# Kernel optimization log

Measured on AMD Instinct MI355X. Metric: run time of the kernel, lower is better.

The kernel has to match this reference:

```python
import jax, jax.numpy as jnp
import numpy as np

N_SRC = 50000
N_DST1 = 20000
N_DST2 = 10000
E1 = 320000
E2 = 160000
T = 12
C_IN = 64
HID = 16
C_OUT = 32


def _gat_layer(src_feat, dst_feat, src_idx, dst_idx, ew, W, a_l, a_r, n_dst):
    # src_feat: [N_src, T, C], dst_feat: [N_dst, T, C]
    h_src = jnp.einsum('ntc,co->nto', src_feat, W)   # [N_src, T, O]
    h_dst = jnp.einsum('ntc,co->nto', dst_feat, W)   # [N_dst, T, O]
    el = jnp.einsum('nto,o->nt', h_src, a_l)          # [N_src, T]
    er = jnp.einsum('nto,o->nt', h_dst, a_r)          # [N_dst, T]
    # per-edge attention logits
    e = jax.nn.leaky_relu(el[src_idx] + er[dst_idx], negative_slope=0.2)  # [E, T]
    # segment softmax over incoming edges of each dst node
    m = jax.ops.segment_max(e, dst_idx, num_segments=n_dst)               # [N_dst, T]
    ex = jnp.exp(e - m[dst_idx])
    s = jax.ops.segment_sum(ex, dst_idx, num_segments=n_dst)
    alpha = ex / (s[dst_idx] + 1e-9)                                      # [E, T]
    msg = (alpha * ew[:, None])[:, :, None] * h_src[src_idx]              # [E, T, O]
    return jax.ops.segment_sum(msg, dst_idx, num_segments=n_dst)          # [N_dst, T, O]


def setup_inputs() -> dict:
    key = jax.random.key(0)
    ks = jax.random.split(key, 12)
    inp = {
        'node_feat': jax.random.normal(ks[0], (T, N_SRC, C_IN), dtype=jnp.float32),
        'edge_src1': jax.random.randint(ks[1], (E1,), 0, N_SRC, dtype=jnp.int32),
        'edge_dst1': jax.random.randint(ks[2], (E1,), 0, N_DST1, dtype=jnp.int32),
        'edge_weight1': jax.random.uniform(ks[3], (E1,), dtype=jnp.float32),
        'edge_src2': jax.random.randint(ks[4], (E2,), 0, N_DST1, dtype=jnp.int32),
        'edge_dst2': jax.random.randint(ks[5], (E2,), 0, N_DST2, dtype=jnp.int32),
        'edge_weight2': jax.random.uniform(ks[6], (E2,), dtype=jnp.float32),
        'W1': jax.random.normal(ks[7], (C_IN, HID), dtype=jnp.float32) * (1.0 / np.sqrt(C_IN)),
        'a_l1': jax.random.normal(ks[8], (HID,), dtype=jnp.float32) * 0.1,
        'a_r1': jax.random.normal(ks[9], (HID,), dtype=jnp.float32) * 0.1,
        'W2': jax.random.normal(ks[10], (HID, C_OUT), dtype=jnp.float32) * (1.0 / np.sqrt(HID)),
        'a_l2': jax.random.normal(ks[11], (C_OUT,), dtype=jnp.float32) * 0.1,
        'a_r2': jax.random.normal(jax.random.fold_in(key, 99), (C_OUT,), dtype=jnp.float32) * 0.1,
    }
    return inp


def reference(node_feat, edge_src1, edge_dst1, edge_weight1,
              edge_src2, edge_dst2, edge_weight2,
              W1, a_l1, a_r1, W2, a_l2, a_r2):
    # [T, N, C] -> [N, T, C]
    x = jnp.transpose(node_feat, (1, 0, 2))
    h1 = _gat_layer(x, x[:N_DST1], edge_src1, edge_dst1, edge_weight1,
                    W1, a_l1, a_r1, N_DST1)
    h1 = jax.nn.leaky_relu(h1, negative_slope=0.01)
    h2 = _gat_layer(h1, h1[:N_DST2], edge_src2, edge_dst2, edge_weight2,
                    W2, a_l2, a_r2, N_DST2)
    h2 = jax.nn.leaky_relu(h2, negative_slope=0.01)
    # [N_dst2, T, O] -> [T, N_dst2, O]
    return jnp.transpose(h2, (1, 0, 2))
```

## Files before the change

### kernel.cpp

```cpp
#include <hip/hip_runtime.h>

#define N_SRC 50000
#define N_DST1 20000
#define N_DST2 10000
#define E1 320000
#define E2 160000
#define T 12
#define C_IN 64
#define HID 16
#define C_OUT 32

__device__ __forceinline__ float lrelu(float x, float s) { return x > 0.f ? x : s * x; }

__device__ __forceinline__ int xcd_swizzle(int p, int W) {
    int x = p & 7, k = p >> 3;
    int q = W >> 3, r = W & 7;
    return (x < r ? x * (q + 1) : r * (q + 1) + (x - r) * q) + k;
}

__global__ __launch_bounds__(256) void k_zero(int4* __restrict__ p, int n4)
{
    int i = blockIdx.x * 256 + threadIdx.x;
    if (i < n4) p[i] = make_int4(0, 0, 0, 0);
}

__global__ __launch_bounds__(256) void k_transform1(
    const float* __restrict__ nf, const float* __restrict__ W1,
    const float* __restrict__ a_l, const float* __restrict__ a_r,
    float* __restrict__ hs1, float* __restrict__ el1, float* __restrict__ er1)
{
    __shared__ float xs[64][68];
    __shared__ float w[C_IN][HID];
    __shared__ float al[HID], ar[HID];
    int tx = threadIdx.x;
    int t = blockIdx.y;
    int n0 = blockIdx.x * 64;
    int nrem = N_SRC - n0; if (nrem > 64) nrem = 64;

    reinterpret_cast<float4*>(&w[0][0])[tx] = reinterpret_cast<const float4*>(W1)[tx];
    if (tx < HID) al[tx] = a_l[tx];
    else if (tx < 2 * HID) ar[tx - HID] = a_r[tx - HID];

    const float4* gp = reinterpret_cast<const float4*>(nf + ((size_t)t * N_SRC + n0) * C_IN);
#pragma unroll
    for (int k = 0; k < 4; k++) {
        int f = k * 256 + tx;
        int node = f >> 4;
        if (node < nrem)
            *reinterpret_cast<float4*>(&xs[node][(f & 15) * 4]) = gp[f];
    }
    __syncthreads();

    int q = tx & 3;
    int nn = tx >> 2;
    float4 acc = make_float4(0.f, 0.f, 0.f, 0.f);
#pragma unroll
    for (int c4 = 0; c4 < 16; c4++) {
        float4 xA = *reinterpret_cast<const float4*>(&xs[nn][c4 * 4]);
        float4 w0 = *reinterpret_cast<const float4*>(&w[c4 * 4 + 0][q * 4]);
        float4 w1 = *reinterpret_cast<const float4*>(&w[c4 * 4 + 1][q * 4]);
        float4 w2 = *reinterpret_cast<const float4*>(&w[c4 * 4 + 2][q * 4]);
        float4 w3 = *reinterpret_cast<const float4*>(&w[c4 * 4 + 3][q * 4]);
        acc.x += xA.x * w0.x + xA.y * w1.x + xA.z * w2.x + xA.w * w3.x;
        acc.y += xA.x * w0.y + xA.y * w1.y + xA.z * w2.y + xA.w * w3.y;
        acc.z += xA.x * w0.z + xA.y * w1.z + xA.z * w2.z + xA.w * w3.z;
        acc.w += xA.x * w0.w + xA.y * w1.w + xA.z * w2.w + xA.w * w3.w;
    }

    float el = acc.x * al[q * 4] + acc.y * al[q * 4 + 1] + acc.z * al[q * 4 + 2] + acc.w * al[q * 4 + 3];
    float er = acc.x * ar[q * 4] + acc.y * ar[q * 4 + 1] + acc.z * ar[q * 4 + 2] + acc.w * ar[q * 4 + 3];
    el += __shfl_xor(el, 1); el += __shfl_xor(el, 2);
    er += __shfl_xor(er, 1); er += __shfl_xor(er, 2);

    if (nn < nrem) {
        float* hb = hs1 + ((size_t)t * N_SRC + n0) * HID;
        *reinterpret_cast<float4*>(hb + (size_t)nn * HID + q * 4) = acc;
        if (q == 0) {
            int n = n0 + nn;
            el1[(size_t)t * N_SRC + n] = el;
            if (n < N_DST1) er1[(size_t)t * N_DST1 + n] = er;
        }
    }
}

__global__ __launch_bounds__(256) void k_hist(
    const int* __restrict__ d1, const int* __restrict__ d2,
    int* __restrict__ cnt1, int* __restrict__ cnt2)
{
    int e = blockIdx.x * 256 + threadIdx.x;
    if (e < E1) atomicAdd(&cnt1[d1[e]], 1);
    else if (e < E1 + E2) atomicAdd(&cnt2[d2[e - E1]], 1);
}

__device__ void scan_one(const int* cnt, int* off, int* cur, int N)
{
    __shared__ int part[1024];
    int tx = threadIdx.x;
    int CH = (N + 1023) / 1024;
    int base = tx * CH;
    int p = 0;
    for (int k = 0; k < CH; k++) { int i = base + k; if (i < N) p += cnt[i]; }
    part[tx] = p;
    __syncthreads();
#pragma unroll
    for (int d = 1; d < 1024; d <<= 1) {
        int v = (tx >= d) ? part[tx - d] : 0;
        __syncthreads();
        part[tx] += v;
        __syncthreads();
    }
    int run = (tx == 0) ? 0 : part[tx - 1];
    if (tx == 0) off[0] = 0;
    for (int k = 0; k < CH; k++) {
        int i = base + k;
        if (i < N) { cur[i] = run; run += cnt[i]; off[i + 1] = run; }
    }
}

__global__ __launch_bounds__(1024) void k_scan(
    const int* __restrict__ cnt1, int* __restrict__ off1, int* __restrict__ cur1,
    const int* __restrict__ cnt2, int* __restrict__ off2, int* __restrict__ cur2,
    const float* __restrict__ W2, const float* __restrict__ al2,
    const float* __restrict__ ar2, float* __restrict__ wl2, float* __restrict__ wr2)
{
    if (blockIdx.x == 2) {
        int tx = threadIdx.x;
        if (tx < 32) {
            int c = tx & 15;
            const float* a = (tx < 16) ? al2 : ar2;
            float s = 0.f;
            for (int o = 0; o < C_OUT; o++) s += W2[c * C_OUT + o] * a[o];
            if (tx < 16) wl2[c] = s; else wr2[c] = s;
        }
        return;
    }
    if (blockIdx.x == 0) scan_one(cnt1, off1, cur1, N_DST1);
    else                 scan_one(cnt2, off2, cur2, N_DST2);
}

__global__ __launch_bounds__(256) void k_scatter(
    const int* __restrict__ s1, const int* __restrict__ d1, const float* __restrict__ w1,
    int* __restrict__ cur1, int2* __restrict__ sw1,
    const int* __restrict__ s2, const int* __restrict__ d2, const float* __restrict__ w2,
    int* __restrict__ cur2, int2* __restrict__ sw2)
{
    int e = blockIdx.x * 256 + threadIdx.x;
    if (e < E1) {
        int d = d1[e];
        int p = atomicAdd(&cur1[d], 1);
        sw1[p] = make_int2(s1[e], __float_as_int(w1[e]));
    } else if (e < E1 + E2) {
        int ee = e - E1;
        int d = d2[ee];
        int p = atomicAdd(&cur2[d], 1);
        sw2[p] = make_int2(s2[ee], __float_as_int(w2[ee]));
    }
}

template <int NDST, int NSRC, bool FINAL>
__global__ __launch_bounds__(256) void k_gat(
    const int* __restrict__ off, const int2* __restrict__ sw,
    const float* __restrict__ el, const float* __restrict__ er,
    const float* __restrict__ hs, float* __restrict__ outp,
    const float* __restrict__ wl, const float* __restrict__ wr,
    float* __restrict__ el_out, float* __restrict__ er_out)
{
    __shared__ float w2s[FINAL ? HID * C_OUT : 1];
    int tx = threadIdx.x;
    if (FINAL) {
        for (int idx = tx; idx < HID * C_OUT; idx += 256) w2s[idx] = wl[idx];
        __syncthreads();
    }
    int wblk = xcd_swizzle(blockIdx.x, (NDST * T) / 16);
    int grp = tx >> 4;
    int lane16 = tx & 15;
    int q = lane16 & 3;
    int eslot = lane16 >> 2;
    int g = wblk * 16 + grp;
    int t = g / NDST;
    int d = g - t * NDST;
    int start = off[d], end = off[d + 1];
    float erv = er[g];
    const float* elb = el + (size_t)t * NSRC;
    const float* hsb = hs + (size_t)t * NSRC * HID;

    float4 num = make_float4(0.f, 0.f, 0.f, 0.f);
    float den = 0.f;
    int i = start + eslot;
    for (; i + 4 < end; i += 8) {
        int2 sa = sw[i];
        int2 sb = sw[i + 4];
        float ea = elb[sa.x];
        float eb = elb[sb.x];
        float4 ha = *reinterpret_cast<const float4*>(hsb + (size_t)sa.x * HID + q * 4);
        float4 hb = *reinterpret_cast<const float4*>(hsb + (size_t)sb.x * HID + q * 4);
        float exa = __expf(lrelu(ea + erv, 0.2f));
        float exb = __expf(lrelu(eb + erv, 0.2f));
        den += exa + exb;
        float ca = exa * __int_as_float(sa.y);
        float cb = exb * __int_as_float(sb.y);
        num.x += ca * ha.x + cb * hb.x;
        num.y += ca * ha.y + cb * hb.y;
        num.z += ca * ha.z + cb * hb.z;
        num.w += ca * ha.w + cb * hb.w;
    }
    if (i < end) {
        int2 sa = sw[i];
        float ea = elb[sa.x];
        float4 ha = *reinterpret_cast<const float4*>(hsb + (size_t)sa.x * HID + q * 4);
        float exa = __expf(lrelu(ea + erv, 0.2f));
        den += exa;
        float ca = exa * __int_as_float(sa.y);
        num.x += ca * ha.x; num.y += ca * ha.y;
        num.z += ca * ha.z; num.w += ca * ha.w;
    }
#pragma unroll
    for (int mk = 4; mk <= 8; mk <<= 1) {
        num.x += __shfl_xor(num.x, mk);
        num.y += __shfl_xor(num.y, mk);
        num.z += __shfl_xor(num.z, mk);
        num.w += __shfl_xor(num.w, mk);
        den   += __shfl_xor(den, mk);
    }
    float inv = 1.f / (den + 1e-9f);
    float4 v = make_float4(num.x * inv, num.y * inv, num.z * inv, num.w * inv);

    if (!FINAL) {
        v.x = lrelu(v.x, 0.01f); v.y = lrelu(v.y, 0.01f);
        v.z = lrelu(v.z, 0.01f); v.w = lrelu(v.w, 0.01f);
        if (eslot == 0) {
            *reinterpret_cast<float4*>(outp + (size_t)g * HID + q * 4) = v;
            float pl = v.x * wl[q * 4] + v.y * wl[q * 4 + 1] + v.z * wl[q * 4 + 2] + v.w * wl[q * 4 + 3];
            float pr = v.x * wr[q * 4] + v.y * wr[q * 4 + 1] + v.z * wr[q * 4 + 2] + v.w * wr[q * 4 + 3];
            pl += __shfl_xor(pl, 1); pl += __shfl_xor(pl, 2);
            pr += __shfl_xor(pr, 1); pr += __shfl_xor(pr, 2);
            if (q == 0) {
                el_out[g] = pl;
                if (d < N_DST2) er_out[(size_t)t * N_DST2 + d] = pr;
            }
        }
    } else {
        float4 v1, v2, v3;
        v1.x = __shfl_xor(v.x, 1); v1.y = __shfl_xor(v.y, 1); v1.z = __shfl_xor(v.z, 1); v1.w = __shfl_xor(v.w, 1);
        v2.x = __shfl_xor(v.x, 2); v2.y = __shfl_xor(v.y, 2); v2.z = __shfl_xor(v.z, 2); v2.w = __shfl_xor(v.w, 2);
        v3.x = __shfl_xor(v.x, 3); v3.y = __shfl_xor(v.y, 3); v3.z = __shfl_xor(v.z, 3); v3.w = __shfl_xor(v.w, 3);
        int obase = q * 8;
        float out8[8];
#pragma unroll
        for (int oo = 0; oo < 8; oo++) out8[oo] = 0.f;
#define ACCQ(Q, R0)                                                             \
        {                                                                       \
            int r0 = (R0) * 4;                                                  \
            _Pragma("unroll")                                                   \
            for (int oo = 0; oo < 8; oo++)                                      \
                out8[oo] += (Q).x * w2s[(r0 + 0) * C_OUT + obase + oo]          \
                          + (Q).y * w2s[(r0 + 1) * C_OUT + obase + oo]          \
                          + (Q).z * w2s[(r0 + 2) * C_OUT + obase + oo]          \
                          + (Q).w * w2s[(r0 + 3) * C_OUT + obase + oo];         \
        }
        ACCQ(v,  q);
        ACCQ(v1, q ^ 1);
        ACCQ(v2, q ^ 2);
        ACCQ(v3, q ^ 3);
#undef ACCQ
        if (eslot == 0) {
            float* op = outp + (size_t)g * C_OUT + obase;
            float4 w0 = make_float4(lrelu(out8[0], 0.01f), lrelu(out8[1], 0.01f),
                                    lrelu(out8[2], 0.01f), lrelu(out8[3], 0.01f));
            float4 w1 = make_float4(lrelu(out8[4], 0.01f), lrelu(out8[5], 0.01f),
                                    lrelu(out8[6], 0.01f), lrelu(out8[7], 0.01f));
            *reinterpret_cast<float4*>(op) = w0;
            *reinterpret_cast<float4*>(op + 4) = w1;
        }
    }
}

extern "C" void kernel_launch(void* const* d_in, const int* in_sizes, int n_in,
                              void* d_out, int out_size, void* d_ws, size_t ws_size,
                              hipStream_t stream)
{
    const float* node_feat = (const float*)d_in[0];
    const int*   esrc1     = (const int*)d_in[1];
    const int*   edst1     = (const int*)d_in[2];
    const float* ew1       = (const float*)d_in[3];
    const int*   esrc2     = (const int*)d_in[4];
    const int*   edst2     = (const int*)d_in[5];
    const float* ew2       = (const float*)d_in[6];
    const float* W1        = (const float*)d_in[7];
    const float* a_l1      = (const float*)d_in[8];
    const float* a_r1      = (const float*)d_in[9];
    const float* W2        = (const float*)d_in[10];
    const float* a_l2      = (const float*)d_in[11];
    const float* a_r2      = (const float*)d_in[12];
    float* out = (float*)d_out;

    float* ws = (float*)d_ws;
    float* hs1 = ws;
    float* el1 = hs1 + 9600000;
    float* er1 = el1 + 600000;
    float* h1  = er1 + 240000;
    float* el2 = h1 + 3840000;
    float* er2 = el2 + 240000;
    float* wl2 = er2 + 120000;
    float* wr2 = wl2 + 16;
    int2* sw1 = (int2*)(wr2 + 16);
    int2* sw2 = sw1 + E1;
    int* cnt1 = (int*)(sw2 + E2);
    int* cnt2 = cnt1 + N_DST1;
    int* off1 = cnt2 + N_DST2;
    int* cur1 = off1 + N_DST1 + 1;
    int* off2 = cur1 + N_DST1;
    int* cur2 = off2 + N_DST2 + 1;

    k_zero<<<30, 256, 0, stream>>>((int4*)cnt1, (N_DST1 + N_DST2) / 4);
    k_hist<<<(E1 + E2 + 255) / 256, 256, 0, stream>>>(edst1, edst2, cnt1, cnt2);
    k_scan<<<3, 1024, 0, stream>>>(cnt1, off1, cur1, cnt2, off2, cur2,
                                   W2, a_l2, a_r2, wl2, wr2);
    k_scatter<<<(E1 + E2 + 255) / 256, 256, 0, stream>>>(
        esrc1, edst1, ew1, cur1, sw1,
        esrc2, edst2, ew2, cur2, sw2);

    {
        dim3 g((N_SRC + 63) / 64, T);
        k_transform1<<<g, 256, 0, stream>>>(node_feat, W1, a_l1, a_r1, hs1, el1, er1);
    }
    k_gat<N_DST1, N_SRC, false><<<(N_DST1 * T) / 16, 256, 0, stream>>>(
        off1, sw1, el1, er1, hs1, h1, wl2, wr2, el2, er2);
    k_gat<N_DST2, N_DST1, true><<<(N_DST2 * T) / 16, 256, 0, stream>>>(
        off2, sw2, el2, er2, h1, out, W2, nullptr, nullptr, nullptr);
}
```

Before: 209.2 us.

## Co-schedule transform tiles with histogram and scatter kernels, unroll GAT edge loop

Splits the per-time-step input transform across the histogram and scatter launches, so that half the time steps run as extra blocks alongside each latency-bound atomic pass and the standalone transform launch is removed. The GAT aggregation loop also gains a 4-edge-per-iteration unrolled main loop, which puts more independent gather loads in flight per lane. Mixing block types within one launch may unbalance scheduling, and the wider unroll raises register pressure.

After: 211.6 us. Within noise of the previous version (+1.1%).

```diff
diff --git a/kernel.cpp b/kernel.cpp
--- a/kernel.cpp
+++ b/kernel.cpp
@@ -9,6 +9,8 @@
 #define C_IN 64
 #define HID 16
 #define C_OUT 32
+#define EB 1875
+#define TB 782
 
 __device__ __forceinline__ float lrelu(float x, float s) { return x > 0.f ? x : s * x; }
 
@@ -24,7 +26,8 @@
     if (i < n4) p[i] = make_int4(0, 0, 0, 0);
 }
 
-__global__ __launch_bounds__(256) void k_transform1(
+__device__ __forceinline__ void transform_tile(
+    int nblk, int t, int tx,
     const float* __restrict__ nf, const float* __restrict__ W1,
     const float* __restrict__ a_l, const float* __restrict__ a_r,
     float* __restrict__ hs1, float* __restrict__ el1, float* __restrict__ er1)
@@ -32,9 +35,7 @@
     __shared__ float xs[64][68];
     __shared__ float w[C_IN][HID];
     __shared__ float al[HID], ar[HID];
-    int tx = threadIdx.x;
-    int t = blockIdx.y;
-    int n0 = blockIdx.x * 64;
+    int n0 = nblk * 64;
     int nrem = N_SRC - n0; if (nrem > 64) nrem = 64;
 
     reinterpret_cast<float4*>(&w[0][0])[tx] = reinterpret_cast<const float4*>(W1)[tx];
@@ -83,13 +84,50 @@
     }
 }
 
-__global__ __launch_bounds__(256) void k_hist(
+__global__ __launch_bounds__(256) void k_A(
     const int* __restrict__ d1, const int* __restrict__ d2,
-    int* __restrict__ cnt1, int* __restrict__ cnt2)
-{
-    int e = blockIdx.x * 256 + threadIdx.x;
-    if (e < E1) atomicAdd(&cnt1[d1[e]], 1);
-    else if (e < E1 + E2) atomicAdd(&cnt2[d2[e - E1]], 1);
+    int* __restrict__ cnt1, int* __restrict__ cnt2,
+    const float* __restrict__ nf, const float* __restrict__ W1,
+    const float* __restrict__ a_l, const float* __restrict__ a_r,
+    float* __restrict__ hs1, float* __restrict__ el1, float* __restrict__ er1)
+{
+    if (blockIdx.x < EB) {
+        int e = blockIdx.x * 256 + threadIdx.x;
+        if (e < E1) atomicAdd(&cnt1[d1[e]], 1);
+        else atomicAdd(&cnt2[d2[e - E1]], 1);
+        return;
+    }
+    int idx = blockIdx.x - EB;
+    transform_tile(idx % TB, idx / TB, threadIdx.x,
+                   nf, W1, a_l, a_r, hs1, el1, er1);
+}
+
+__global__ __launch_bounds__(256) void k_B(
+    const int* __restrict__ s1, const int* __restrict__ d1, const float* __restrict__ w1,
+    int* __restrict__ cur1, int2* __restrict__ sw1,
+    const int* __restrict__ s2, const int* __restrict__ d2, const float* __restrict__ w2,
+    int* __restrict__ cur2, int2* __restrict__ sw2,
+    const float* __restrict__ nf, const float* __restrict__ W1,
+    const float* __restrict__ a_l, const float* __restrict__ a_r,
+    float* __restrict__ hs1, float* __restrict__ el1, float* __restrict__ er1)
+{
+    if (blockIdx.x < EB) {
+        int e = blockIdx.x * 256 + threadIdx.x;
+        if (e < E1) {
+            int d = d1[e];
+            int p = atomicAdd(&cur1[d], 1);
+            sw1[p] = make_int2(s1[e], __float_as_int(w1[e]));
+        } else {
+            int ee = e - E1;
+            int d = d2[ee];
+            int p = atomicAdd(&cur2[d], 1);
+            sw2[p] = make_int2(s2[ee], __float_as_int(w2[ee]));
+        }
+        return;
+    }
+    int idx = blockIdx.x - EB;
+    transform_tile(idx % TB, 6 + idx / TB, threadIdx.x,
+                   nf, W1, a_l, a_r, hs1, el1, er1);
 }
 
 __device__ void scan_one(const int* cnt, int* off, int* cur, int N)
@@ -138,24 +176,17 @@
     else                 scan_one(cnt2, off2, cur2, N_DST2);
 }
 
-__global__ __launch_bounds__(256) void k_scatter(
-    const int* __restrict__ s1, const int* __restrict__ d1, const float* __restrict__ w1,
-    int* __restrict__ cur1, int2* __restrict__ sw1,
-    const int* __restrict__ s2, const int* __restrict__ d2, const float* __restrict__ w2,
-    int* __restrict__ cur2, int2* __restrict__ sw2)
-{
-    int e = blockIdx.x * 256 + threadIdx.x;
-    if (e < E1) {
-        int d = d1[e];
-        int p = atomicAdd(&cur1[d], 1);
-        sw1[p] = make_int2(s1[e], __float_as_int(w1[e]));
-    } else if (e < E1 + E2) {
-        int ee = e - E1;
-        int d = d2[ee];
-        int p = atomicAdd(&cur2[d], 1);
-        sw2[p] = make_int2(s2[ee], __float_as_int(w2[ee]));
-    }
-}
+#define EDGE1(I)                                                                \
+    {                                                                           \
+        int2 sa = sw[I];                                                        \
+        float ea = elb[sa.x];                                                   \
+        float4 ha = *reinterpret_cast<const float4*>(hsb + (size_t)sa.x * HID + q * 4); \
+        float exa = __expf(lrelu(ea + erv, 0.2f));                              \
+        den += exa;                                                             \
+        float ca = exa * __int_as_float(sa.y);                                  \
+        num.x += ca * ha.x; num.y += ca * ha.y;                                 \
+        num.z += ca * ha.z; num.w += ca * ha.w;                                 \
+    }
 
 template <int NDST, int NSRC, bool FINAL>
 __global__ __launch_bounds__(256) void k_gat(
@@ -187,6 +218,33 @@
     float4 num = make_float4(0.f, 0.f, 0.f, 0.f);
     float den = 0.f;
     int i = start + eslot;
+    for (; i + 12 < end; i += 16) {
+        int2 sa = sw[i];
+        int2 sb = sw[i + 4];
+        int2 sc = sw[i + 8];
+        int2 sd = sw[i + 12];
+        float ea = elb[sa.x];
+        float eb = elb[sb.x];
+        float ec = elb[sc.x];
+        float ed = elb[sd.x];
+        float4 ha = *reinterpret_cast<const float4*>(hsb + (size_t)sa.x * HID + q * 4);
+        float4 hb = *reinterpret_cast<const float4*>(hsb + (size_t)sb.x * HID + q * 4);
+        float4 hc = *reinterpret_cast<const float4*>(hsb + (size_t)sc.x * HID + q * 4);
+        float4 hd = *reinterpret_cast<const float4*>(hsb + (size_t)sd.x * HID + q * 4);
+        float exa = __expf(lrelu(ea + erv, 0.2f));
+        float exb = __expf(lrelu(eb + erv, 0.2f));
+        float exc = __expf(lrelu(ec + erv, 0.2f));
+        float exd = __expf(lrelu(ed + erv, 0.2f));
+        den += (exa + exb) + (exc + exd);
+        float ca = exa * __int_as_float(sa.y);
+        float cb = exb * __int_as_float(sb.y);
+        float cc = exc * __int_as_float(sc.y);
+        float cd = exd * __int_as_float(sd.y);
+        num.x += ca * ha.x + cb * hb.x + cc * hc.x + cd * hd.x;
+        num.y += ca * ha.y + cb * hb.y + cc * hc.y + cd * hd.y;
+        num.z += ca * ha.z + cb * hb.z + cc * hc.z + cd * hd.z;
+        num.w += ca * ha.w + cb * hb.w + cc * hc.w + cd * hd.w;
+    }
     for (; i + 4 < end; i += 8) {
         int2 sa = sw[i];
         int2 sb = sw[i + 4];
@@ -204,16 +262,7 @@
         num.z += ca * ha.z + cb * hb.z;
         num.w += ca * ha.w + cb * hb.w;
     }
-    if (i < end) {
-        int2 sa = sw[i];
-        float ea = elb[sa.x];
-        float4 ha = *reinterpret_cast<const float4*>(hsb + (size_t)sa.x * HID + q * 4);
-        float exa = __expf(lrelu(ea + erv, 0.2f));
-        den += exa;
-        float ca = exa * __int_as_float(sa.y);
-        num.x += ca * ha.x; num.y += ca * ha.y;
-        num.z += ca * ha.z; num.w += ca * ha.w;
-    }
+    if (i < end) EDGE1(i);
 #pragma unroll
     for (int mk = 4; mk <= 8; mk <<= 1) {
         num.x += __shfl_xor(num.x, mk);
@@ -313,17 +362,13 @@
     int* cur2 = off2 + N_DST2 + 1;
 
     k_zero<<<30, 256, 0, stream>>>((int4*)cnt1, (N_DST1 + N_DST2) / 4);
-    k_hist<<<(E1 + E2 + 255) / 256, 256, 0, stream>>>(edst1, edst2, cnt1, cnt2);
+    k_A<<<EB + TB * 6, 256, 0, stream>>>(edst1, edst2, cnt1, cnt2,
+                                         node_feat, W1, a_l1, a_r1, hs1, el1, er1);
     k_scan<<<3, 1024, 0, stream>>>(cnt1, off1, cur1, cnt2, off2, cur2,
                                    W2, a_l2, a_r2, wl2, wr2);
-    k_scatter<<<(E1 + E2 + 255) / 256, 256, 0, stream>>>(
-        esrc1, edst1, ew1, cur1, sw1,
-        esrc2, edst2, ew2, cur2, sw2);
-
-    {
-        dim3 g((N_SRC + 63) / 64, T);
-        k_transform1<<<g, 256, 0, stream>>>(node_feat, W1, a_l1, a_r1, hs1, el1, er1);
-    }
+    k_B<<<EB + TB * 6, 256, 0, stream>>>(esrc1, edst1, ew1, cur1, sw1,
+                                         esrc2, edst2, ew2, cur2, sw2,
+                                         node_feat, W1, a_l1, a_r1, hs1, el1, er1);
     k_gat<N_DST1, N_SRC, false><<<(N_DST1 * T) / 16, 256, 0, stream>>>(
         off1, sw1, el1, er1, hs1, h1, wl2, wr2, el2, er2);
     k_gat<N_DST2, N_DST1, true><<<(N_DST2 * T) / 16, 256, 0, stream>>>(
```

## Map one wavefront per destination node with all timesteps across lanes

Applied to the files above, without the earlier changes.

Changes the GAT aggregation work mapping. Before, a 16-lane group handled one (t,d) pair, with edges split across 4 slots and reduced by shuffles. Now each 64-lane wavefront handles one destination node, and lanes cover the 12 timesteps times 4 feature quarters. Each lane walks every edge sequentially with 4-way unrolled loads. The aim is to share the edge-list (sw) loads across timesteps and drop the cross-slot shuffle reductions. In exchange, 16 of the 64 lanes sit idle, and the per-lane serial edge chain gets longer.

Measured after the change: 264.8 us. +26.6%, slower.

```diff
diff --git a/kernel.cpp b/kernel.cpp
--- a/kernel.cpp
+++ b/kernel.cpp
@@ -171,25 +171,62 @@
         for (int idx = tx; idx < HID * C_OUT; idx += 256) w2s[idx] = wl[idx];
         __syncthreads();
     }
-    int wblk = xcd_swizzle(blockIdx.x, (NDST * T) / 16);
-    int grp = tx >> 4;
-    int lane16 = tx & 15;
-    int q = lane16 & 3;
-    int eslot = lane16 >> 2;
-    int g = wblk * 16 + grp;
-    int t = g / NDST;
-    int d = g - t * NDST;
+    int wblk = xcd_swizzle(blockIdx.x, NDST / 4);
+    int wave = tx >> 6;
+    int lane = tx & 63;
+    int t = lane >> 2;
+    int q = lane & 3;
+    int d = wblk * 4 + wave;
+    bool act = t < T;
+    int tt = act ? t : 0;
     int start = off[d], end = off[d + 1];
-    float erv = er[g];
-    const float* elb = el + (size_t)t * NSRC;
-    const float* hsb = hs + (size_t)t * NSRC * HID;
+    float erv = er[(size_t)tt * NDST + d];
+    const float* elb = el + (size_t)tt * NSRC;
+    const float* hsb = hs + (size_t)tt * NSRC * HID;
 
     float4 num = make_float4(0.f, 0.f, 0.f, 0.f);
     float den = 0.f;
-    int i = start + eslot;
-    for (; i + 4 < end; i += 8) {
+    int i = start;
+#define GEDGE(SA)                                                               \
+        {                                                                       \
+            float e_ = elb[SA.x];                                               \
+            float4 h_ = *reinterpret_cast<const float4*>(hsb + (size_t)SA.x * HID + q * 4); \
+            float ex_ = __expf(lrelu(e_ + erv, 0.2f));                          \
+            den += ex_;                                                         \
+            float c_ = ex_ * __int_as_float(SA.y);                              \
+            num.x += c_ * h_.x; num.y += c_ * h_.y;                             \
+            num.z += c_ * h_.z; num.w += c_ * h_.w;                             \
+        }
+    for (; i + 3 < end; i += 4) {
         int2 sa = sw[i];
-        int2 sb = sw[i + 4];
+        int2 sb = sw[i + 1];
+        int2 sc = sw[i + 2];
+        int2 sd = sw[i + 3];
+        float ea = elb[sa.x];
+        float eb = elb[sb.x];
+        float ec = elb[sc.x];
+        float ed = elb[sd.x];
+        float4 ha = *reinterpret_cast<const float4*>(hsb + (size_t)sa.x * HID + q * 4);
+        float4 hb = *reinterpret_cast<const float4*>(hsb + (size_t)sb.x * HID + q * 4);
+        float4 hc = *reinterpret_cast<const float4*>(hsb + (size_t)sc.x * HID + q * 4);
+        float4 hd = *reinterpret_cast<const float4*>(hsb + (size_t)sd.x * HID + q * 4);
+        float exa = __expf(lrelu(ea + erv, 0.2f));
+        float exb = __expf(lrelu(eb + erv, 0.2f));
+        float exc = __expf(lrelu(ec + erv, 0.2f));
+        float exd = __expf(lrelu(ed + erv, 0.2f));
+        den += (exa + exb) + (exc + exd);
+        float ca = exa * __int_as_float(sa.y);
+        float cb = exb * __int_as_float(sb.y);
+        float cc = exc * __int_as_float(sc.y);
+        float cd = exd * __int_as_float(sd.y);
+        num.x += ca * ha.x + cb * hb.x + cc * hc.x + cd * hd.x;
+        num.y += ca * ha.y + cb * hb.y + cc * hc.y + cd * hd.y;
+        num.z += ca * ha.z + cb * hb.z + cc * hc.z + cd * hd.z;
+        num.w += ca * ha.w + cb * hb.w + cc * hc.w + cd * hd.w;
+    }
+    for (; i + 1 < end; i += 2) {
+        int2 sa = sw[i];
+        int2 sb = sw[i + 1];
         float ea = elb[sa.x];
         float eb = elb[sb.x];
         float4 ha = *reinterpret_cast<const float4*>(hsb + (size_t)sa.x * HID + q * 4);
@@ -206,29 +243,18 @@
     }
     if (i < end) {
         int2 sa = sw[i];
-        float ea = elb[sa.x];
-        float4 ha = *reinterpret_cast<const float4*>(hsb + (size_t)sa.x * HID + q * 4);
-        float exa = __expf(lrelu(ea + erv, 0.2f));
-        den += exa;
-        float ca = exa * __int_as_float(sa.y);
-        num.x += ca * ha.x; num.y += ca * ha.y;
-        num.z += ca * ha.z; num.w += ca * ha.w;
-    }
-#pragma unroll
-    for (int mk = 4; mk <= 8; mk <<= 1) {
-        num.x += __shfl_xor(num.x, mk);
-        num.y += __shfl_xor(num.y, mk);
-        num.z += __shfl_xor(num.z, mk);
-        num.w += __shfl_xor(num.w, mk);
-        den   += __shfl_xor(den, mk);
-    }
+        GEDGE(sa);
+    }
+#undef GEDGE
+
     float inv = 1.f / (den + 1e-9f);
     float4 v = make_float4(num.x * inv, num.y * inv, num.z * inv, num.w * inv);
 
     if (!FINAL) {
-        v.x = lrelu(v.x, 0.01f); v.y = lrelu(v.y, 0.01f);
-        v.z = lrelu(v.z, 0.01f); v.w = lrelu(v.w, 0.01f);
-        if (eslot == 0) {
+        if (act) {
+            v.x = lrelu(v.x, 0.01f); v.y = lrelu(v.y, 0.01f);
+            v.z = lrelu(v.z, 0.01f); v.w = lrelu(v.w, 0.01f);
+            int g = tt * NDST + d;
             *reinterpret_cast<float4*>(outp + (size_t)g * HID + q * 4) = v;
             float pl = v.x * wl[q * 4] + v.y * wl[q * 4 + 1] + v.z * wl[q * 4 + 2] + v.w * wl[q * 4 + 3];
             float pr = v.x * wr[q * 4] + v.y * wr[q * 4 + 1] + v.z * wr[q * 4 + 2] + v.w * wr[q * 4 + 3];
@@ -236,34 +262,35 @@
             pr += __shfl_xor(pr, 1); pr += __shfl_xor(pr, 2);
             if (q == 0) {
                 el_out[g] = pl;
-                if (d < N_DST2) er_out[(size_t)t * N_DST2 + d] = pr;
+                if (d < N_DST2) er_out[(size_t)tt * N_DST2 + d] = pr;
             }
         }
     } else {
-        float4 v1, v2, v3;
-        v1.x = __shfl_xor(v.x, 1); v1.y = __shfl_xor(v.y, 1); v1.z = __shfl_xor(v.z, 1); v1.w = __shfl_xor(v.w, 1);
-        v2.x = __shfl_xor(v.x, 2); v2.y = __shfl_xor(v.y, 2); v2.z = __shfl_xor(v.z, 2); v2.w = __shfl_xor(v.w, 2);
-        v3.x = __shfl_xor(v.x, 3); v3.y = __shfl_xor(v.y, 3); v3.z = __shfl_xor(v.z, 3); v3.w = __shfl_xor(v.w, 3);
-        int obase = q * 8;
-        float out8[8];
+        if (act) {
+            float4 v1, v2, v3;
+            v1.x = __shfl_xor(v.x, 1); v1.y = __shfl_xor(v.y, 1); v1.z = __shfl_xor(v.z, 1); v1.w = __shfl_xor(v.w, 1);
+            v2.x = __shfl_xor(v.x, 2); v2.y = __shfl_xor(v.y, 2); v2.z = __shfl_xor(v.z, 2); v2.w = __shfl_xor(v.w, 2);
+            v3.x = __shfl_xor(v.x, 3); v3.y = __shfl_xor(v.y, 3); v3.z = __shfl_xor(v.z, 3); v3.w = __shfl_xor(v.w, 3);
+            int obase = q * 8;
+            float out8[8];
 #pragma unroll
-        for (int oo = 0; oo < 8; oo++) out8[oo] = 0.f;
+            for (int oo = 0; oo < 8; oo++) out8[oo] = 0.f;
 #define ACCQ(Q, R0)                                                             \
-        {                                                                       \
-            int r0 = (R0) * 4;                                                  \
-            _Pragma("unroll")                                                   \
-            for (int oo = 0; oo < 8; oo++)                                      \
-                out8[oo] += (Q).x * w2s[(r0 + 0) * C_OUT + obase + oo]          \
-                          + (Q).y * w2s[(r0 + 1) * C_OUT + obase + oo]          \
-                          + (Q).z * w2s[(r0 + 2) * C_OUT + obase + oo]          \
-                          + (Q).w * w2s[(r0 + 3) * C_OUT + obase + oo];         \
-        }
-        ACCQ(v,  q);
-        ACCQ(v1, q ^ 1);
-        ACCQ(v2, q ^ 2);
-        ACCQ(v3, q ^ 3);
+            {                                                                   \
+                int r0 = (R0) * 4;                                              \
+                _Pragma("unroll")                                               \
+                for (int oo = 0; oo < 8; oo++)                                  \
+                    out8[oo] += (Q).x * w2s[(r0 + 0) * C_OUT + obase + oo]      \
+                              + (Q).y * w2s[(r0 + 1) * C_OUT + obase + oo]      \
+                              + (Q).z * w2s[(r0 + 2) * C_OUT + obase + oo]      \
+                              + (Q).w * w2s[(r0 + 3) * C_OUT + obase + oo];     \
+            }
+            ACCQ(v,  q);
+            ACCQ(v1, q ^ 1);
+            ACCQ(v2, q ^ 2);
+            ACCQ(v3, q ^ 3);
 #undef ACCQ
-        if (eslot == 0) {
+            int g = tt * NDST + d;
             float* op = outp + (size_t)g * C_OUT + obase;
             float4 w0 = make_float4(lrelu(out8[0], 0.01f), lrelu(out8[1], 0.01f),
                                     lrelu(out8[2], 0.01f), lrelu(out8[3], 0.01f));
@@ -324,8 +351,8 @@
         dim3 g((N_SRC + 63) / 64, T);
         k_transform1<<<g, 256, 0, stream>>>(node_feat, W1, a_l1, a_r1, hs1, el1, er1);
     }
-    k_gat<N_DST1, N_SRC, false><<<(N_DST1 * T) / 16, 256, 0, stream>>>(
+    k_gat<N_DST1, N_SRC, false><<<N_DST1 / 4, 256, 0, stream>>>(
         off1, sw1, el1, er1, hs1, h1, wl2, wr2, el2, er2);
-    k_gat<N_DST2, N_DST1, true><<<(N_DST2 * T) / 16, 256, 0, stream>>>(
+    k_gat<N_DST2, N_DST1, true><<<N_DST2 / 4, 256, 0, stream>>>(
         off2, sw2, el2, er2, h1, out, W2, nullptr, nullptr, nullptr);
 }
```

## Store layer-1 hidden features in fp16 and unroll edge gather by four

Applied to the files above, without the earlier changes.

The layer-1 transformed source features are written as half precision, which halves their footprint (from about 38MB to 19MB) and the bytes gathered per edge in the first GAT kernel. The aggregation loop also gains a 4-way unrolled stage so more independent gathers are in flight per thread. Half precision adds rounding error to the hidden features, though the attention logits stay in fp32.

Result: no change. 207.0 us (-1.1%).

```diff
diff --git a/kernel.cpp b/kernel.cpp
--- a/kernel.cpp
+++ b/kernel.cpp
@@ -1,4 +1,5 @@
 #include <hip/hip_runtime.h>
+#include <hip/hip_fp16.h>
 
 #define N_SRC 50000
 #define N_DST1 20000
@@ -10,6 +11,8 @@
 #define HID 16
 #define C_OUT 32
 
+struct H4 { __half2 a, b; };
+
 __device__ __forceinline__ float lrelu(float x, float s) { return x > 0.f ? x : s * x; }
 
 __device__ __forceinline__ int xcd_swizzle(int p, int W) {
@@ -18,6 +21,19 @@
     return (x < r ? x * (q + 1) : r * (q + 1) + (x - r) * q) + k;
 }
 
+template <bool HALF>
+__device__ __forceinline__ float4 load_h(const void* base, int s, int q) {
+    if (HALF) {
+        const __half* p = (const __half*)base + (size_t)s * HID + q * 4;
+        H4 hv = *reinterpret_cast<const H4*>(p);
+        float2 lo = __half22float2(hv.a);
+        float2 hi = __half22float2(hv.b);
+        return make_float4(lo.x, lo.y, hi.x, hi.y);
+    } else {
+        return *reinterpret_cast<const float4*>((const float*)base + (size_t)s * HID + q * 4);
+    }
+}
+
 __global__ __launch_bounds__(256) void k_zero(int4* __restrict__ p, int n4)
 {
     int i = blockIdx.x * 256 + threadIdx.x;
@@ -27,7 +43,7 @@
 __global__ __launch_bounds__(256) void k_transform1(
     const float* __restrict__ nf, const float* __restrict__ W1,
     const float* __restrict__ a_l, const float* __restrict__ a_r,
-    float* __restrict__ hs1, float* __restrict__ el1, float* __restrict__ er1)
+    __half* __restrict__ hs1, float* __restrict__ el1, float* __restrict__ er1)
 {
     __shared__ float xs[64][68];
     __shared__ float w[C_IN][HID];
@@ -73,8 +89,11 @@
     er += __shfl_xor(er, 1); er += __shfl_xor(er, 2);
 
     if (nn < nrem) {
-        float* hb = hs1 + ((size_t)t * N_SRC + n0) * HID;
-        *reinterpret_cast<float4*>(hb + (size_t)nn * HID + q * 4) = acc;
+        __half* hb = hs1 + ((size_t)t * N_SRC + n0) * HID;
+        H4 pk;
+        pk.a = __floats2half2_rn(acc.x, acc.y);
+        pk.b = __floats2half2_rn(acc.z, acc.w);
+        *reinterpret_cast<H4*>(hb + (size_t)nn * HID + q * 4) = pk;
         if (q == 0) {
             int n = n0 + nn;
             el1[(size_t)t * N_SRC + n] = el;
@@ -157,11 +176,11 @@
     }
 }
 
-template <int NDST, int NSRC, bool FINAL>
+template <int NDST, int NSRC, bool FINAL, bool HHS>
 __global__ __launch_bounds__(256) void k_gat(
     const int* __restrict__ off, const int2* __restrict__ sw,
     const float* __restrict__ el, const float* __restrict__ er,
-    const float* __restrict__ hs, float* __restrict__ outp,
+    const void* __restrict__ hs, float* __restrict__ outp,
     const float* __restrict__ wl, const float* __restrict__ wr,
     float* __restrict__ el_out, float* __restrict__ er_out)
 {
@@ -182,18 +201,47 @@
     int start = off[d], end = off[d + 1];
     float erv = er[g];
     const float* elb = el + (size_t)t * NSRC;
-    const float* hsb = hs + (size_t)t * NSRC * HID;
+    const void* hsb = HHS
+        ? (const void*)((const __half*)hs + (size_t)t * NSRC * HID)
+        : (const void*)((const float*)hs + (size_t)t * NSRC * HID);
 
     float4 num = make_float4(0.f, 0.f, 0.f, 0.f);
     float den = 0.f;
     int i = start + eslot;
+    for (; i + 12 < end; i += 16) {
+        int2 sa = sw[i];
+        int2 sb = sw[i + 4];
+        int2 sc = sw[i + 8];
+        int2 sd = sw[i + 12];
+        float ea = elb[sa.x];
+        float eb = elb[sb.x];
+        float ec = elb[sc.x];
+        float ed = elb[sd.x];
+        float4 ha = load_h<HHS>(hsb, sa.x, q);
+        float4 hb = load_h<HHS>(hsb, sb.x, q);
+        float4 hc = load_h<HHS>(hsb, sc.x, q);
+        float4 hd = load_h<HHS>(hsb, sd.x, q);
+        float exa = __expf(lrelu(ea + erv, 0.2f));
+        float exb = __expf(lrelu(eb + erv, 0.2f));
+        float exc = __expf(lrelu(ec + erv, 0.2f));
+        float exd = __expf(lrelu(ed + erv, 0.2f));
+        den += (exa + exb) + (exc + exd);
+        float ca = exa * __int_as_float(sa.y);
+        float cb = exb * __int_as_float(sb.y);
+        float cc = exc * __int_as_float(sc.y);
+        float cd = exd * __int_as_float(sd.y);
+        num.x += ca * ha.x + cb * hb.x + cc * hc.x + cd * hd.x;
+        num.y += ca * ha.y + cb * hb.y + cc * hc.y + cd * hd.y;
+        num.z += ca * ha.z + cb * hb.z + cc * hc.z + cd * hd.z;
+        num.w += ca * ha.w + cb * hb.w + cc * hc.w + cd * hd.w;
+    }
     for (; i + 4 < end; i += 8) {
         int2 sa = sw[i];
         int2 sb = sw[i + 4];
         float ea = elb[sa.x];
         float eb = elb[sb.x];
-        float4 ha = *reinterpret_cast<const float4*>(hsb + (size_t)sa.x * HID + q * 4);
-        float4 hb = *reinterpret_cast<const float4*>(hsb + (size_t)sb.x * HID + q * 4);
+        float4 ha = load_h<HHS>(hsb, sa.x, q);
+        float4 hb = load_h<HHS>(hsb, sb.x, q);
         float exa = __expf(lrelu(ea + erv, 0.2f));
         float exb = __expf(lrelu(eb + erv, 0.2f));
         den += exa + exb;
@@ -207,7 +255,7 @@
     if (i < end) {
         int2 sa = sw[i];
         float ea = elb[sa.x];
-        float4 ha = *reinterpret_cast<const float4*>(hsb + (size_t)sa.x * HID + q * 4);
+        float4 ha = load_h<HHS>(hsb, sa.x, q);
         float exa = __expf(lrelu(ea + erv, 0.2f));
         den += exa;
         float ca = exa * __int_as_float(sa.y);
@@ -295,8 +343,8 @@
     float* out = (float*)d_out;
 
     float* ws = (float*)d_ws;
-    float* hs1 = ws;
-    float* el1 = hs1 + 9600000;
+    __half* hs1 = (__half*)ws;
+    float* el1 = ws + 4800000;
     float* er1 = el1 + 600000;
     float* h1  = er1 + 240000;
     float* el2 = h1 + 3840000;
@@ -324,8 +372,8 @@
         dim3 g((N_SRC + 63) / 64, T);
         k_transform1<<<g, 256, 0, stream>>>(node_feat, W1, a_l1, a_r1, hs1, el1, er1);
     }
-    k_gat<N_DST1, N_SRC, false><<<(N_DST1 * T) / 16, 256, 0, stream>>>(
+    k_gat<N_DST1, N_SRC, false, true><<<(N_DST1 * T) / 16, 256, 0, stream>>>(
         off1, sw1, el1, er1, hs1, h1, wl2, wr2, el2, er2);
-    k_gat<N_DST2, N_DST1, true><<<(N_DST2 * T) / 16, 256, 0, stream>>>(
+    k_gat<N_DST2, N_DST1, true, false><<<(N_DST2 * T) / 16, 256, 0, stream>>>(
         off2, sw2, el2, er2, h1, out, W2, nullptr, nullptr, nullptr);
 }
```
